# Performance work log

Measured on AMD Instinct MI355X. Metric: run time of the kernel, lower is better.

Reference implementation:

```python
import jax, jax.numpy as jnp
import numpy as np

LN2 = float(np.log(2.0))

def ssp(x):
    # ShiftedSoftplus: softplus(x) - log(2)
    return jax.nn.softplus(x) - LN2

N_NODES = 40000
N_EDGES = 640000
HIDDEN = 128
N_FILTERS = 128
N_GAUSS = 50
CUTOFF = 10.0

def setup_inputs() -> dict:
    key = jax.random.key(0)
    ks = jax.random.split(key, 12)
    s = 0.05
    x = jax.random.normal(ks[0], (N_NODES, HIDDEN), dtype=jnp.float32)
    edge_index = jax.random.randint(ks[1], (2, N_EDGES), 0, N_NODES)
    edge_weight = jax.random.uniform(ks[2], (N_EDGES,), dtype=jnp.float32) * CUTOFF
    edge_attr = jax.random.normal(ks[3], (N_EDGES, N_GAUSS), dtype=jnp.float32)
    # filter MLP params (Linear(num_gaussians,num_filters), ssp, Linear(num_filters,num_filters))
    mlp_w1 = jax.random.normal(ks[4], (N_FILTERS, N_GAUSS), dtype=jnp.float32) * s
    mlp_b1 = jnp.zeros((N_FILTERS,), dtype=jnp.float32)
    mlp_w2 = jax.random.normal(ks[5], (N_FILTERS, N_FILTERS), dtype=jnp.float32) * s
    mlp_b2 = jnp.zeros((N_FILTERS,), dtype=jnp.float32)
    # CFConv linears: lin1 (no bias), lin2 (bias)
    lin1_w = jax.random.normal(ks[6], (N_FILTERS, HIDDEN), dtype=jnp.float32) * s
    lin2_w = jax.random.normal(ks[7], (HIDDEN, N_FILTERS), dtype=jnp.float32) * s
    lin2_b = jnp.zeros((HIDDEN,), dtype=jnp.float32)
    # output linear
    lin_w = jax.random.normal(ks[8], (HIDDEN, HIDDEN), dtype=jnp.float32) * s
    lin_b = jnp.zeros((HIDDEN,), dtype=jnp.float32)
    return {
        "x": x, "edge_index": edge_index, "edge_weight": edge_weight, "edge_attr": edge_attr,
        "mlp_w1": mlp_w1, "mlp_b1": mlp_b1, "mlp_w2": mlp_w2, "mlp_b2": mlp_b2,
        "lin1_w": lin1_w, "lin2_w": lin2_w, "lin2_b": lin2_b,
        "lin_w": lin_w, "lin_b": lin_b,
    }

def reference(x, edge_index, edge_weight, edge_attr,
              mlp_w1, mlp_b1, mlp_w2, mlp_b2,
              lin1_w, lin2_w, lin2_b, lin_w, lin_b):
    src, dst = edge_index[0], edge_index[1]
    # cosine envelope
    C = 0.5 * (jnp.cos(edge_weight * jnp.pi / CUTOFF) + 1.0)  # (E,)
    # filter MLP on Gaussian-smeared distances
    W = ssp(edge_attr @ mlp_w1.T + mlp_b1) @ mlp_w2.T + mlp_b2  # (E, F)
    W = W * C[:, None]
    # CFConv: lin1 -> gather x_j -> multiply -> scatter-add -> lin2
    h = x @ lin1_w.T                                            # (N, F)
    msg = h[src] * W                                            # (E, F)
    agg = jax.ops.segment_sum(msg, dst, num_segments=x.shape[0])  # (N, F)
    h2 = agg @ lin2_w.T + lin2_b                                # (N, H)
    # activation + output projection
    out = ssp(h2) @ lin_w.T + lin_b                             # (N, H)
    return out
```

## Files before the change

### kernel.cpp

```cpp
#include <hip/hip_runtime.h>
#include <math.h>

#define LN2F 0.69314718055994531f

typedef _Float16 v8hf __attribute__((ext_vector_type(8)));
typedef float    v4f  __attribute__((ext_vector_type(4)));

__device__ __forceinline__ float ssp_fast(float x) {
    float e = __expf(-fabsf(x));
    return fmaxf(x, 0.f) + __logf(1.f + e) - LN2F;
}

__global__ __launch_bounds__(256)
void prep_kernel(const float* __restrict__ w1, const float* __restrict__ w2,
                 const float* __restrict__ l1w, const float* __restrict__ l2w,
                 const float* __restrict__ lw,
                 _Float16* __restrict__ w1f, _Float16* __restrict__ w2f,
                 _Float16* __restrict__ l1f, _Float16* __restrict__ l2f,
                 _Float16* __restrict__ lwf)
{
    int idx = blockIdx.x * 256 + threadIdx.x;
    if (idx < 8192) {
        int i = idx & 7, lane = (idx >> 3) & 63, ks = (idx >> 9) & 1, nt = idx >> 10;
        int r = nt * 16 + (lane & 15);
        int k = ks * 32 + (lane >> 4) * 8 + i;
        w1f[idx] = (k < 50) ? (_Float16)w1[r * 50 + k] : (_Float16)0.f;
        return;
    }
    int o = idx - 8192;
    if (o >= 4 * 16384) return;
    int which = o >> 14;
    int p = o & 16383;
    int i = p & 7, lane = (p >> 3) & 63, ks = (p >> 9) & 3, nt = p >> 11;
    int r = nt * 16 + (lane & 15);
    int k = ks * 32 + (lane >> 4) * 8 + i;
    const float* src = (which == 0) ? w2 : (which == 1) ? l1w : (which == 2) ? l2w : lw;
    _Float16* dst   = (which == 0) ? w2f : (which == 1) ? l1f : (which == 2) ? l2f : lwf;
    dst[p] = (_Float16)src[r * 128 + k];
}

__global__ __launch_bounds__(256)
void h_gemm_kernel(const float* __restrict__ X, const _Float16* __restrict__ Wf,
                   float* __restrict__ Y, int M)
{
    const int tid = threadIdx.x, lane = tid & 63, wv = tid >> 6;
    const int l15 = lane & 15, quad = lane >> 4;
    const int mb = blockIdx.x * 64 + wv * 16;

    const int mA = (mb + l15 < M) ? (mb + l15) : (M - 1);
    v8hf a[4];
    #pragma unroll
    for (int ks = 0; ks < 4; ++ks) {
        const float4* xp = (const float4*)&X[(size_t)mA * 128 + ks * 32 + quad * 8];
        float4 x0 = xp[0], x1 = xp[1];
        v8hf t = {(_Float16)x0.x, (_Float16)x0.y, (_Float16)x0.z, (_Float16)x0.w,
                  (_Float16)x1.x, (_Float16)x1.y, (_Float16)x1.z, (_Float16)x1.w};
        a[ks] = t;
    }
    #pragma unroll
    for (int nt = 0; nt < 8; ++nt) {
        v4f acc = {0.f, 0.f, 0.f, 0.f};
        #pragma unroll
        for (int ks = 0; ks < 4; ++ks) {
            const v8hf b = *(const v8hf*)&Wf[((nt * 4 + ks) * 64 + lane) * 8];
            acc = __builtin_amdgcn_mfma_f32_16x16x32_f16(a[ks], b, acc, 0, 0, 0);
        }
        const int col = nt * 16 + l15;
        #pragma unroll
        for (int r = 0; r < 4; ++r) {
            int row = mb + quad * 4 + r;
            if (row < M) Y[(size_t)row * 128 + col] = acc[r];
        }
    }
}

__global__ __launch_bounds__(256)
void fused_out_kernel(const float* __restrict__ agg, const _Float16* __restrict__ l2f,
                      const float* __restrict__ l2b, const _Float16* __restrict__ lwf,
                      const float* __restrict__ lb, float* __restrict__ out, int M)
{
    __shared__ __align__(16) _Float16 Sh[64 * 138];
    const int tid = threadIdx.x, lane = tid & 63, wv = tid >> 6;
    const int l15 = lane & 15, quad = lane >> 4;
    const int m0 = wv * 16;
    const int gbase = blockIdx.x * 64;

    const int mA = (gbase + m0 + l15 < M) ? (gbase + m0 + l15) : (M - 1);
    v8hf a[4];
    #pragma unroll
    for (int ks = 0; ks < 4; ++ks) {
        const float4* xp = (const float4*)&agg[(size_t)mA * 128 + ks * 32 + quad * 8];
        float4 x0 = xp[0], x1 = xp[1];
        v8hf t = {(_Float16)x0.x, (_Float16)x0.y, (_Float16)x0.z, (_Float16)x0.w,
                  (_Float16)x1.x, (_Float16)x1.y, (_Float16)x1.z, (_Float16)x1.w};
        a[ks] = t;
    }
    #pragma unroll
    for (int nt = 0; nt < 8; ++nt) {
        v4f acc = {0.f, 0.f, 0.f, 0.f};
        #pragma unroll
        for (int ks = 0; ks < 4; ++ks) {
            const v8hf b = *(const v8hf*)&l2f[((nt * 4 + ks) * 64 + lane) * 8];
            acc = __builtin_amdgcn_mfma_f32_16x16x32_f16(a[ks], b, acc, 0, 0, 0);
        }
        const float bj = l2b[nt * 16 + l15];
        #pragma unroll
        for (int r = 0; r < 4; ++r)
            Sh[(m0 + quad * 4 + r) * 138 + nt * 16 + l15] =
                (_Float16)ssp_fast(acc[r] + bj);
    }
    v8hf ua[4];
    #pragma unroll
    for (int ks = 0; ks < 4; ++ks)
        ua[ks] = *(const v8hf*)&Sh[(m0 + l15) * 138 + ks * 32 + quad * 8];

    #pragma unroll
    for (int nt = 0; nt < 8; ++nt) {
        v4f acc = {0.f, 0.f, 0.f, 0.f};
        #pragma unroll
        for (int ks = 0; ks < 4; ++ks) {
            const v8hf b = *(const v8hf*)&lwf[((nt * 4 + ks) * 64 + lane) * 8];
            acc = __builtin_amdgcn_mfma_f32_16x16x32_f16(ua[ks], b, acc, 0, 0, 0);
        }
        const int col = nt * 16 + l15;
        const float bj = lb[col];
        #pragma unroll
        for (int r = 0; r < 4; ++r) {
            int row = gbase + m0 + quad * 4 + r;
            if (row < M) out[(size_t)row * 128 + col] = acc[r] + bj;
        }
    }
}

__global__ __launch_bounds__(256, 5)
void edge_kernel(const float* __restrict__ attr,
                 const float* __restrict__ ew,
                 const int* __restrict__ srcI,
                 const int* __restrict__ dstI,
                 const _Float16* __restrict__ w1f,
                 const _Float16* __restrict__ w2f,
                 const float* __restrict__ b1,
                 const float* __restrict__ b2,
                 const float* __restrict__ h,
                 float* __restrict__ agg,
                 int E)
{
    __shared__ __align__(16) _Float16 Af[64 * 64];
    __shared__ __align__(16) _Float16 Uh[64 * 138];

    const int tid = threadIdx.x;
    const int e_base = blockIdx.x * 64;
    const int lane = tid & 63, wv = tid >> 6;
    const int m0 = wv * 16, l15 = lane & 15, quad = lane >> 4;

    float cC[4]; const float* hrow[4]; float* arow[4]; bool val[4];
    #pragma unroll
    for (int r = 0; r < 4; ++r) {
        int eg = e_base + m0 + quad * 4 + r;
        val[r] = eg < E;
        int e = val[r] ? eg : (E - 1);
        cC[r] = 0.5f * (__cosf(ew[e] * 0.31415926535897932f) + 1.f);
        hrow[r] = h + (size_t)srcI[e] * 128;
        arow[r] = agg + (size_t)dstI[e] * 128;
    }

    for (int idx = tid; idx < 4096; idx += 256) {
        int r = idx >> 6, g = idx & 63;
        int e = e_base + r;
        float v = (g < 50 && e < E) ? attr[(size_t)e * 50 + g] : 0.f;
        Af[((((r >> 4) * 2 + (g >> 5)) * 64) + (((g & 31) >> 3) * 16) + (r & 15)) * 8
           + (g & 7)] = (_Float16)v;
    }
    __syncthreads();

    float hv[8][4];
    #pragma unroll
    for (int nt = 0; nt < 8; ++nt)
        #pragma unroll
        for (int r = 0; r < 4; ++r)
            hv[nt][r] = hrow[r][nt * 16 + l15];

    const v8hf a0 = *(const v8hf*)&Af[((wv * 2 + 0) * 64 + lane) * 8];
    const v8hf a1 = *(const v8hf*)&Af[((wv * 2 + 1) * 64 + lane) * 8];
    #pragma unroll
    for (int nt = 0; nt < 8; ++nt) {
        v4f acc = {0.f, 0.f, 0.f, 0.f};
        const v8hf bA = *(const v8hf*)&w1f[((nt * 2 + 0) * 64 + lane) * 8];
        const v8hf bB = *(const v8hf*)&w1f[((nt * 2 + 1) * 64 + lane) * 8];
        acc = __builtin_amdgcn_mfma_f32_16x16x32_f16(a0, bA, acc, 0, 0, 0);
        acc = __builtin_amdgcn_mfma_f32_16x16x32_f16(a1, bB, acc, 0, 0, 0);
        const float bj = b1[nt * 16 + l15];
        #pragma unroll
        for (int r = 0; r < 4; ++r)
            Uh[(m0 + quad * 4 + r) * 138 + nt * 16 + l15] =
                (_Float16)ssp_fast(acc[r] + bj);
    }

    v8hf ua[4];
    #pragma unroll
    for (int ks = 0; ks < 4; ++ks)
        ua[ks] = *(const v8hf*)&Uh[(m0 + l15) * 138 + ks * 32 + quad * 8];

    #pragma unroll
    for (int nt = 0; nt < 8; ++nt) {
        v4f acc = {0.f, 0.f, 0.f, 0.f};
        #pragma unroll
        for (int ks = 0; ks < 4; ++ks) {
            const v8hf b = *(const v8hf*)&w2f[((nt * 4 + ks) * 64 + lane) * 8];
            acc = __builtin_amdgcn_mfma_f32_16x16x32_f16(ua[ks], b, acc, 0, 0, 0);
        }
        const int col = nt * 16 + l15;
        const float bj = b2[col];
        #pragma unroll
        for (int r = 0; r < 4; ++r) {
            if (val[r]) {
                float wf = (acc[r] + bj) * cC[r];
                atomicAdd(&arow[r][col], wf * hv[nt][r]);
            }
        }
    }
}

extern "C" void kernel_launch(void* const* d_in, const int* in_sizes, int n_in,
                              void* d_out, int out_size, void* d_ws, size_t ws_size,
                              hipStream_t stream)
{
    const float* x   = (const float*)d_in[0];
    const int*   ei  = (const int*)  d_in[1];
    const float* ew  = (const float*)d_in[2];
    const float* ea  = (const float*)d_in[3];
    const float* w1  = (const float*)d_in[4];
    const float* b1  = (const float*)d_in[5];
    const float* w2  = (const float*)d_in[6];
    const float* b2  = (const float*)d_in[7];
    const float* l1w = (const float*)d_in[8];
    const float* l2w = (const float*)d_in[9];
    const float* l2b = (const float*)d_in[10];
    const float* lw  = (const float*)d_in[11];
    const float* lb  = (const float*)d_in[12];

    const int N = in_sizes[0] / 128;
    const int E = in_sizes[2];

    float* hbuf = (float*)d_ws;
    float* agg  = hbuf + (size_t)N * 128;
    _Float16* w1f = (_Float16*)(agg + (size_t)N * 128);
    _Float16* w2f = w1f + 8192;
    _Float16* l1f = w2f + 16384;
    _Float16* l2f = l1f + 16384;
    _Float16* lwf = l2f + 16384;

    const int nb = (N + 63) / 64;

    prep_kernel<<<288, 256, 0, stream>>>(w1, w2, l1w, l2w, lw,
                                         w1f, w2f, l1f, l2f, lwf);
    hipMemsetAsync(agg, 0, (size_t)N * 128 * sizeof(float), stream);
    h_gemm_kernel<<<nb, 256, 0, stream>>>(x, l1f, hbuf, N);
    edge_kernel<<<(E + 63) / 64, 256, 0, stream>>>(ea, ew, ei, ei + E,
                                                   w1f, w2f, b1, b2, hbuf, agg, E);
    fused_out_kernel<<<nb, 256, 0, stream>>>(agg, l2f, l2b, lwf, lb, (float*)d_out, N);
}
```

Measured before the change: 546.4 us.

## Load edge attrs straight to registers, split node GEMMs over columns, raise occupancy

```diff
diff --git a/kernel.cpp b/kernel.cpp
--- a/kernel.cpp
+++ b/kernel.cpp
@@ -46,6 +46,7 @@
     const int tid = threadIdx.x, lane = tid & 63, wv = tid >> 6;
     const int l15 = lane & 15, quad = lane >> 4;
     const int mb = blockIdx.x * 64 + wv * 16;
+    const int nt0 = blockIdx.y * 4;
 
     const int mA = (mb + l15 < M) ? (mb + l15) : (M - 1);
     v8hf a[4];
@@ -58,7 +59,7 @@
         a[ks] = t;
     }
     #pragma unroll
-    for (int nt = 0; nt < 8; ++nt) {
+    for (int nt = nt0; nt < nt0 + 4; ++nt) {
         v4f acc = {0.f, 0.f, 0.f, 0.f};
         #pragma unroll
         for (int ks = 0; ks < 4; ++ks) {
@@ -84,6 +85,7 @@
     const int l15 = lane & 15, quad = lane >> 4;
     const int m0 = wv * 16;
     const int gbase = blockIdx.x * 64;
+    const int nt0 = blockIdx.y * 4;
 
     const int mA = (gbase + m0 + l15 < M) ? (gbase + m0 + l15) : (M - 1);
     v8hf a[4];
@@ -115,7 +117,7 @@
         ua[ks] = *(const v8hf*)&Sh[(m0 + l15) * 138 + ks * 32 + quad * 8];
 
     #pragma unroll
-    for (int nt = 0; nt < 8; ++nt) {
+    for (int nt = nt0; nt < nt0 + 4; ++nt) {
         v4f acc = {0.f, 0.f, 0.f, 0.f};
         #pragma unroll
         for (int ks = 0; ks < 4; ++ks) {
@@ -132,7 +134,7 @@
     }
 }
 
-__global__ __launch_bounds__(256, 5)
+__global__ __launch_bounds__(256, 7)
 void edge_kernel(const float* __restrict__ attr,
                  const float* __restrict__ ew,
                  const int* __restrict__ srcI,
@@ -145,7 +147,6 @@
                  float* __restrict__ agg,
                  int E)
 {
-    __shared__ __align__(16) _Float16 Af[64 * 64];
     __shared__ __align__(16) _Float16 Uh[64 * 138];
 
     const int tid = threadIdx.x;
@@ -164,14 +165,32 @@
         arow[r] = agg + (size_t)dstI[e] * 128;
     }
 
-    for (int idx = tid; idx < 4096; idx += 256) {
-        int r = idx >> 6, g = idx & 63;
-        int e = e_base + r;
-        float v = (g < 50 && e < E) ? attr[(size_t)e * 50 + g] : 0.f;
-        Af[((((r >> 4) * 2 + (g >> 5)) * 64) + (((g & 31) >> 3) * 16) + (r & 15)) * 8
-           + (g & 7)] = (_Float16)v;
-    }
-    __syncthreads();
+    int ar = e_base + m0 + l15;
+    if (ar >= E) ar = E - 1;
+    const float* rp = attr + (size_t)ar * 50;
+    v8hf a0, a1;
+    {
+        const float2 q0 = *(const float2*)(rp + quad * 8 + 0);
+        const float2 q1 = *(const float2*)(rp + quad * 8 + 2);
+        const float2 q2 = *(const float2*)(rp + quad * 8 + 4);
+        const float2 q3 = *(const float2*)(rp + quad * 8 + 6);
+        v8hf t = {(_Float16)q0.x, (_Float16)q0.y, (_Float16)q1.x, (_Float16)q1.y,
+                  (_Float16)q2.x, (_Float16)q2.y, (_Float16)q3.x, (_Float16)q3.y};
+        a0 = t;
+    }
+    {
+        const int cb = 32 + quad * 8;
+        float2 q[4];
+        #pragma unroll
+        for (int j = 0; j < 4; ++j) {
+            const int c = cb + 2 * j;
+            if (c < 50) q[j] = *(const float2*)(rp + c);
+            else        { q[j].x = 0.f; q[j].y = 0.f; }
+        }
+        v8hf t = {(_Float16)q[0].x, (_Float16)q[0].y, (_Float16)q[1].x, (_Float16)q[1].y,
+                  (_Float16)q[2].x, (_Float16)q[2].y, (_Float16)q[3].x, (_Float16)q[3].y};
+        a1 = t;
+    }
 
     float hv[8][4];
     #pragma unroll
@@ -180,8 +199,6 @@
         for (int r = 0; r < 4; ++r)
             hv[nt][r] = hrow[r][nt * 16 + l15];
 
-    const v8hf a0 = *(const v8hf*)&Af[((wv * 2 + 0) * 64 + lane) * 8];
-    const v8hf a1 = *(const v8hf*)&Af[((wv * 2 + 1) * 64 + lane) * 8];
     #pragma unroll
     for (int nt = 0; nt < 8; ++nt) {
         v4f acc = {0.f, 0.f, 0.f, 0.f};
@@ -251,12 +268,14 @@
     _Float16* lwf = l2f + 16384;
 
     const int nb = (N + 63) / 64;
+    const int eb = (E + 63) / 64;
 
     prep_kernel<<<288, 256, 0, stream>>>(w1, w2, l1w, l2w, lw,
                                          w1f, w2f, l1f, l2f, lwf);
     hipMemsetAsync(agg, 0, (size_t)N * 128 * sizeof(float), stream);
-    h_gemm_kernel<<<nb, 256, 0, stream>>>(x, l1f, hbuf, N);
-    edge_kernel<<<(E + 63) / 64, 256, 0, stream>>>(ea, ew, ei, ei + E,
-                                                   w1f, w2f, b1, b2, hbuf, agg, E);
-    fused_out_kernel<<<nb, 256, 0, stream>>>(agg, l2f, l2b, lwf, lb, (float*)d_out, N);
-}
+    h_gemm_kernel<<<dim3(nb, 2), 256, 0, stream>>>(x, l1f, hbuf, N);
+    edge_kernel<<<eb, 256, 0, stream>>>(ea, ew, ei, ei + E, w1f, w2f, b1, b2,
+                                        hbuf, agg, E);
+    fused_out_kernel<<<dim3(nb, 2), 256, 0, stream>>>(agg, l2f, l2b, lwf, lb,
+                                                      (float*)d_out, N);
+}
```

Measured after the change: 543.4 us. Within noise of the previous version (-0.6%).
